# Kernel tuning notes

Measured on AMD Instinct MI355X. Metric: run time of the kernel, lower is better.

## Reference

```python
import jax, jax.numpy as jnp
import numpy as np
import math

B, T, C, NH, LEVEL = 2, 2048, 1024, 16, 3


def _build_sets(T, level):
    # hierarchical dyadic sets: levels `level`..floor(log2(T)), step 2^l
    sets = []
    levelmax = int(math.floor(math.log2(T)))
    for l in range(level, levelmax + 1):
        step = 2 ** l
        for i in range(T // step):
            sets.append((i * step, (i + 1) * step - 1))
    b = np.asarray(sets, dtype=np.int32)
    return b[:, 0], b[:, 1]


def setup_inputs() -> dict:
    key = jax.random.key(0)
    kx, kw1, kw2 = jax.random.split(key, 3)
    x = jax.random.normal(kx, (B, T, C), dtype=jnp.float32)
    # torch nn.Linear stores weight as (out_features, in_features); y = x @ W.T
    W_attn = jax.random.normal(kw1, (3 * C, C), dtype=jnp.float32) * (C ** -0.5)
    W_proj = jax.random.normal(kw2, (C, C), dtype=jnp.float32) * (C ** -0.5)
    return {"x": x, "W_attn": W_attn, "W_proj": W_proj}


def _get_slice(xc, l_idx, r_idx):
    # xc: (B,NH,T,hs) cumulative sums; returns sum over [l_idx, r_idx]
    r = xc[:, :, r_idx, :]
    l = xc[:, :, l_idx - 1, :] * (l_idx >= 1)[None, None, :, None].astype(xc.dtype)
    return r - l


def _forward(x, W_attn, W_proj):
    hs = C // NH
    scale = hs ** -0.5
    qkv = x @ W_attn.T                      # (B,T,3C)
    q, k, v = jnp.split(qkv, 3, axis=2)
    heads = lambda t: t.reshape(B, T, NH, hs).transpose(0, 2, 1, 3)  # (B,NH,T,hs)
    q, k, v = heads(q), heads(k), heads(v)
    phi = lambda t: jax.nn.elu(t) + 1.0     # feature_map = 'elu_plus'
    q_phi, k_phi = phi(q), phi(k)
    k_cum = jnp.cumsum(k_phi, axis=2)
    v_cum = jnp.cumsum(v, axis=2)

    l_np, r_np = _build_sets(T, LEVEL)
    l_idx, r_idx = jnp.asarray(l_np), jnp.asarray(r_np)
    K = _get_slice(k_cum, l_idx, r_idx)     # (B,NH,S,hs)
    V = _get_slice(v_cum, l_idx, r_idx)

    t_idx = jnp.arange(T)
    mask = t_idx[:, None] >= r_idx[None, :]                 # (T,S)
    logits = jnp.einsum('bhtd,bhsd->bhts', q, K) * scale    # raw q here (as in source)
    logits = jnp.where(mask[None, None], logits, -jnp.inf)

    # tail term over last (t mod 2^level)+1 tokens, uses q_phi
    Lmin = 2 ** LEVEL
    tail_len = t_idx % Lmin + 1
    l_tail = t_idx - tail_len + 1
    K_tail = _get_slice(k_cum, l_tail, t_idx)               # (B,NH,T,hs)
    V_tail = _get_slice(v_cum, l_tail, t_idx)
    tail_logit = jnp.sum(q_phi * K_tail, axis=-1) * scale   # (B,NH,T)

    full = jnp.concatenate([logits, tail_logit[..., None]], axis=-1)
    att = jax.nn.softmax(full, axis=-1)
    out = jnp.einsum('bhts,bhsd->bhtd', att[..., :-1], V) + att[..., -1:] * V_tail
    out = out.transpose(0, 2, 1, 3).reshape(B, T, C)
    return out @ W_proj.T


def reference(x, W_attn, W_proj):
    return _forward(x, W_attn, W_proj)
```

## Files before the change

kernel.cpp:

```cpp
#include <hip/hip_runtime.h>
#include <hip/hip_bf16.h>
#include <stdint.h>

#define B_    2
#define T_    2048
#define CD    1024
#define NH_   16
#define HS_   64
#define NSETS 511
#define NSP   512
#define QKV_LD 3072
#define NEGBIG (-3.4e38f)

typedef __attribute__((ext_vector_type(8))) short  short8;
typedef __attribute__((ext_vector_type(4))) float  f32x4;

__device__ __forceinline__ unsigned short f2bf(float f) {
  unsigned u = __float_as_uint(f);
  unsigned r = 0x7FFFu + ((u >> 16) & 1u);
  return (unsigned short)((u + r) >> 16);
}
__device__ __forceinline__ float bf2f(unsigned short h) {
  return __uint_as_float(((unsigned)h) << 16);
}
__device__ __forceinline__ float elu1(float x) {
  return x > 0.f ? x + 1.f : __expf(x);
}
__device__ __forceinline__ void gload16(const unsigned short* g, short* l) {
  __builtin_amdgcn_global_load_lds(
      (const __attribute__((address_space(1))) unsigned int*)g,
      (__attribute__((address_space(3))) unsigned int*)l, 16, 0, 0);
}

__global__ __launch_bounds__(256) void split3_kernel(
    const float* __restrict__ x, const float* __restrict__ Wa,
    const float* __restrict__ Wp,
    unsigned short* __restrict__ xh, unsigned short* __restrict__ xl,
    unsigned short* __restrict__ wah, unsigned short* __restrict__ wal,
    unsigned short* __restrict__ wph) {
  int bid = blockIdx.x;
  const float* src; unsigned short *hi, *lo; int base;
  if (bid < 16384)      { src = x;  hi = xh;  lo = xl;  base = bid; }
  else if (bid < 24576) { src = Wa; hi = wah; lo = wal; base = bid - 16384; }
  else if (bid < 28672) { src = Wa; hi = wah; lo = nullptr; base = bid - 16384; }
  else                  { src = Wp; hi = wph; lo = nullptr; base = bid - 28672; }
  int i = base * 256 + threadIdx.x;
  float v = src[i];
  unsigned short h = f2bf(v);
  hi[i] = h;
  if (lo) lo[i] = f2bf(v - bf2f(h));
}

template<int SPLIT>
__global__ __launch_bounds__(256) void gemm_bt(
    const unsigned short* __restrict__ Ah, const unsigned short* __restrict__ Al,
    const unsigned short* __restrict__ Bh, const unsigned short* __restrict__ Bl,
    float* __restrict__ Cmat, int M, int N, int K, int ldc)
{
  constexpr int NT = SPLIT ? 4 : 2;
  __shared__ short lds[NT * 4096];

  const int nwg = gridDim.x;
  const int cpx = nwg >> 3;
  const int bid = blockIdx.x;
  const int swb = (bid & 7) * cpx + (bid >> 3);
  const int nbx = N >> 7;
  const int bx = swb % nbx;
  const int by = swb / nbx;

  const int row0 = by * 128;
  const int col0 = bx * 128;
  const int tid  = threadIdx.x;
  const int lane = tid & 63;
  const int w    = tid >> 6;
  const int wr   = w >> 1, wc = w & 1;

  f32x4 acc[4][4];
  #pragma unroll
  for (int a = 0; a < 4; ++a)
    #pragma unroll
    for (int b = 0; b < 4; ++b)
      acc[a][b] = (f32x4){0.f, 0.f, 0.f, 0.f};

  const int rlane = lane & 15;
  const int kgrp  = lane >> 4;
  const int rsw   = (kgrp ^ (rlane & 3) ^ ((rlane >> 2) & 3)) << 4;

  const int slr = lane >> 2;
  const int sch = (lane & 3) ^ (slr & 3) ^ ((slr >> 2) & 3);

  const unsigned short* ssrc;
  size_t srb;
  short* sbase;
  if (SPLIT) {
    ssrc = (w == 0) ? Ah : (w == 1) ? Bh : (w == 2) ? Al : Bl;
    srb  = (w & 1) ? (size_t)col0 : (size_t)row0;
    sbase = &lds[w * 4096];
  } else {
    ssrc = (w & 1) ? Bh : Ah;
    srb  = (w & 1) ? (size_t)col0 : (size_t)row0;
    sbase = &lds[(w & 1) * 4096 + (w >> 1) * 2048];
    srb += (size_t)(w >> 1) * 64;
  }

  for (int kt = 0; kt < K; kt += 32) {
    __syncthreads();
    const unsigned short* g0 = ssrc + (srb + slr) * K + kt + (sch << 3);
    if (SPLIT) {
      #pragma unroll
      for (int i = 0; i < 8; ++i)
        gload16(g0 + (size_t)i * 16 * K, sbase + i * 512);
    } else {
      #pragma unroll
      for (int i = 0; i < 4; ++i)
        gload16(g0 + (size_t)i * 16 * K, sbase + i * 512);
    }
    __syncthreads();

    short8 aH[4], bH[4], aL[4], bL[4];
    #pragma unroll
    for (int m = 0; m < 4; ++m) {
      int r    = wr * 64 + m * 16 + rlane;
      int cidx = wc * 64 + m * 16 + rlane;
      aH[m] = *(const short8*)((const char*)lds + r * 64 + rsw);
      bH[m] = *(const short8*)((const char*)lds + 8192 + cidx * 64 + rsw);
      if (SPLIT) {
        aL[m] = *(const short8*)((const char*)lds + 16384 + r * 64 + rsw);
        bL[m] = *(const short8*)((const char*)lds + 24576 + cidx * 64 + rsw);
      }
    }
    #pragma unroll
    for (int mm = 0; mm < 4; ++mm)
      #pragma unroll
      for (int nn = 0; nn < 4; ++nn) {
        acc[mm][nn] = __builtin_amdgcn_mfma_f32_16x16x32_bf16(aH[mm], bH[nn], acc[mm][nn], 0, 0, 0);
        if (SPLIT) {
          acc[mm][nn] = __builtin_amdgcn_mfma_f32_16x16x32_bf16(aH[mm], bL[nn], acc[mm][nn], 0, 0, 0);
          acc[mm][nn] = __builtin_amdgcn_mfma_f32_16x16x32_bf16(aL[mm], bH[nn], acc[mm][nn], 0, 0, 0);
        }
      }
  }

  const int rl = (lane >> 4) * 4;
  const int cl = lane & 15;
  #pragma unroll
  for (int mm = 0; mm < 4; ++mm)
    #pragma unroll
    for (int nn = 0; nn < 4; ++nn)
      #pragma unroll
      for (int r = 0; r < 4; ++r) {
        int row = row0 + wr * 64 + mm * 16 + rl + r;
        int col = col0 + wc * 64 + nn * 16 + cl;
        Cmat[(size_t)row * ldc + col] = acc[mm][nn][r];
      }
}

__global__ __launch_bounds__(256) void cs_part(const float* __restrict__ qkv,
                                               float* __restrict__ part) {
  int blk = blockIdx.x;
  int q   = blk & 1;
  int seg = (blk >> 1) & 31;
  int b   = blk >> 6;
  int c   = threadIdx.x * 4;
  const float* src = qkv + (size_t)(b * T_ + seg * 64) * QKV_LD + CD + q * CD + c;
  float4 s = {0.f, 0.f, 0.f, 0.f};
  #pragma unroll 4
  for (int j = 0; j < 64; ++j) {
    float4 v = *(const float4*)(src + (size_t)j * QKV_LD);
    if (q == 0) {
      s.x += elu1(v.x); s.y += elu1(v.y); s.z += elu1(v.z); s.w += elu1(v.w);
    } else {
      s.x += v.x; s.y += v.y; s.z += v.z; s.w += v.w;
    }
  }
  *(float4*)(part + ((size_t)(b * 32 + seg) * 2048) + q * 1024 + c) = s;
}

__global__ void cs_prefix(float* __restrict__ part) {
  int idx = blockIdx.x * 256 + threadIdx.x;
  int b  = idx >> 11;
  int cc = idx & 2047;
  float run = 0.f;
  #pragma unroll 8
  for (int s = 0; s < 32; ++s) {
    size_t o = (size_t)(b * 32 + s) * 2048 + cc;
    float t = part[o];
    part[o] = run;
    run += t;
  }
}

__global__ __launch_bounds__(256) void cs_final(const float* __restrict__ qkv,
                                                const float* __restrict__ part,
                                                float* __restrict__ kcum,
                                                float* __restrict__ vcum) {
  int blk = blockIdx.x;
  int q   = blk & 1;
  int seg = (blk >> 1) & 31;
  int b   = blk >> 6;
  int c   = threadIdx.x * 4;
  int h   = c >> 6, d = c & 63;
  const float* src = qkv + (size_t)(b * T_ + seg * 64) * QKV_LD + CD + q * CD + c;
  float* dst = (q == 0 ? kcum : vcum) + ((size_t)(b * NH_ + h) * T_ + seg * 64) * HS_ + d;
  float4 s = *(const float4*)(part + ((size_t)(b * 32 + seg) * 2048) + q * 1024 + c);
  #pragma unroll 4
  for (int j = 0; j < 64; ++j) {
    float4 v = *(const float4*)(src + (size_t)j * QKV_LD);
    if (q == 0) {
      s.x += elu1(v.x); s.y += elu1(v.y); s.z += elu1(v.z); s.w += elu1(v.w);
    } else {
      s.x += v.x; s.y += v.y; s.z += v.z; s.w += v.w;
    }
    *(float4*)(dst + (size_t)j * HS_) = s;
  }
}

__global__ void build_sets(const float* __restrict__ kcum, const float* __restrict__ vcum,
                           unsigned short* __restrict__ Ksh, unsigned short* __restrict__ Ksl,
                           float* __restrict__ Vs, int* __restrict__ r_srt) {
  int idx = blockIdx.x * 256 + threadIdx.x;
  if (idx >= B_ * NH_ * NSP * HS_) return;
  int d  = idx & 63;
  int s  = (idx >> 6) & (NSP - 1);
  int bh = idx >> (6 + 9);
  if (s == NSETS) {
    size_t o = ((size_t)(bh << 9) + s) * HS_ + d;
    Ksh[o] = 0; Ksl[o] = 0; Vs[o] = 0.f;
    if (bh == 0 && d == 0) r_srt[s] = 0x7fffffff;
    return;
  }
  int lvl = 3, base = 0;
  while (s >= base + (T_ >> lvl)) { base += T_ >> lvl; ++lvl; }
  int i  = s - base;
  int m  = (i + 1) << lvl;
  int r  = m - 1;
  int li = i << lvl;
  int rank = lvl - 3;
  #pragma unroll
  for (int j = 3; j <= 11; ++j) rank += (m - 8) >> j;

  size_t rowr = ((size_t)bh * T_ + r) * HS_ + d;
  float kr = kcum[rowr], vr = vcum[rowr];
  if (li > 0) {
    size_t rowl = ((size_t)bh * T_ + li - 1) * HS_ + d;
    kr -= kcum[rowl];
    vr -= vcum[rowl];
  }
  size_t o = ((size_t)(bh << 9) + rank) * HS_ + d;
  unsigned short kh = f2bf(kr);
  Ksh[o] = kh;
  Ksl[o] = f2bf(kr - bf2f(kh));
  Vs[o]  = vr;
  if (bh == 0 && d == 0) r_srt[rank] = r;
}

__global__ __launch_bounds__(256) void vst_transpose(
    const float* __restrict__ Vs, unsigned short* __restrict__ Vst) {
  __shared__ float tile[64][65];
  int bh = blockIdx.x >> 3;
  int s0 = (blockIdx.x & 7) * 64;
  int tid = threadIdx.x;
  int srow = tid >> 2, c0 = (tid & 3) * 16;
  const float* src = Vs + ((size_t)(bh << 9) + s0 + srow) * HS_ + c0;
  #pragma unroll
  for (int j = 0; j < 4; ++j) {
    float4 v = *(const float4*)(src + j * 4);
    tile[srow][c0 + j*4 + 0] = v.x; tile[srow][c0 + j*4 + 1] = v.y;
    tile[srow][c0 + j*4 + 2] = v.z; tile[srow][c0 + j*4 + 3] = v.w;
  }
  __syncthreads();
  int d = tid >> 2, sq = (tid & 3) * 16;
  short8 a, b;
  #pragma unroll
  for (int j = 0; j < 8; ++j) {
    a[j] = (short)f2bf(tile[sq + j][d]);
    b[j] = (short)f2bf(tile[sq + 8 + j][d]);
  }
  unsigned short* dst = Vst + ((size_t)(bh << 6) + d) * NSP + s0 + sq;
  *(short8*)dst = a;
  *(short8*)(dst + 8) = b;
}

__global__ __launch_bounds__(256) void attn_mfma(
    const float* __restrict__ qkv, const float* __restrict__ kcum,
    const float* __restrict__ vcum,
    const unsigned short* __restrict__ Ksh, const unsigned short* __restrict__ Ksl,
    const unsigned short* __restrict__ Vst, const int* __restrict__ r_srt,
    unsigned short* __restrict__ attnb)
{
  __shared__ short Qh[64 * 64];
  __shared__ short Ql[64 * 64];
  __shared__ short Pl[4 * 16 * 64];
  __shared__ short KV[3 * 4096];
  __shared__ int   rs_lds[NSP];

  const int blk = blockIdx.x;
  const int xcd = blk & 7;
  const int j   = blk >> 3;
  const int bh  = xcd * 4 + (j >> 5);
  const int tch = (j + ((j >> 5) << 3)) & 31;
  const int b = bh >> 4, h = bh & 15;
  const int t0 = tch * 64;
  const int tid = threadIdx.x;
  const int lane = tid & 63;
  const int w = tid >> 6;
  const int col = lane & 15;
  const float scale = 0.125f;

  const int srow = lane >> 3;
  const int scsw = ((lane & 7) ^ srow) * 8;

  auto stage_tile = [&](short* kv, int s0) {
    #pragma unroll
    for (int L = w * 6; L < w * 6 + 6; ++L) {
      int a = L >> 3, i = L & 7;
      const unsigned short* src;
      if (a == 0)      src = Ksh + ((size_t)(bh << 9) + s0 + i * 8 + srow) * 64 + scsw;
      else if (a == 1) src = Ksl + ((size_t)(bh << 9) + s0 + i * 8 + srow) * 64 + scsw;
      else             src = Vst + ((size_t)(bh << 6) + i * 8 + srow) * NSP + s0 + scsw;
      gload16(src, kv + a * 4096 + i * 512 + lane * 8);
    }
  };

  int nmax = 0;
  #pragma unroll
  for (int jj = 3; jj <= 11; ++jj) nmax += (t0 + 64) >> jj;
  const int ntiles = (nmax + 63) >> 6;

  {
    int row = tid >> 2;
    int d0  = (tid & 3) * 16;
    const float* qr = qkv + (size_t)(b * T_ + t0 + row) * QKV_LD + h * HS_ + d0;
    float qv[16];
    #pragma unroll
    for (int jj = 0; jj < 4; ++jj) {
      float4 v = *(const float4*)(qr + jj * 4);
      qv[jj*4+0] = v.x; qv[jj*4+1] = v.y; qv[jj*4+2] = v.z; qv[jj*4+3] = v.w;
    }
    short8 hh[2], ll[2];
    #pragma unroll
    for (int c = 0; c < 2; ++c)
      #pragma unroll
      for (int jj = 0; jj < 8; ++jj) {
        float f = qv[c*8+jj];
        unsigned short hi = f2bf(f);
        hh[c][jj] = (short)hi;
        ll[c][jj] = (short)f2bf(f - bf2f(hi));
      }
    int swz = (row & 7) << 4;
    #pragma unroll
    for (int c = 0; c < 2; ++c) {
      int addr = (row * 128 + d0 * 2 + c * 16) ^ swz;
      *(short8*)((char*)Qh + addr) = hh[c];
      *(short8*)((char*)Ql + addr) = ll[c];
    }
    for (int s = tid; s < NSP; s += 256) rs_lds[s] = r_srt[s];
  }

  int rows[4];
  #pragma unroll
  for (int r = 0; r < 4; ++r) rows[r] = t0 + w * 16 + (lane >> 4) * 4 + r;

  f32x4 O[4];
  #pragma unroll
  for (int f = 0; f < 4; ++f) O[f] = (f32x4){0.f, 0.f, 0.f, 0.f};
  float mrun[4] = {NEGBIG, NEGBIG, NEGBIG, NEGBIG};
  float lsum[4] = {0.f, 0.f, 0.f, 0.f};

  const int arow  = w * 16 + col;
  const int aswz  = (arow & 7) << 4;
  const int kgrp  = (lane >> 4) * 8;

  for (int tile = 0; tile < ntiles; ++tile) {
    const int s0 = tile * 64;
    stage_tile(KV, s0);
    __syncthreads();

    const char* kc = (const char*)KV;
    f32x4 S[4];
    #pragma unroll
    for (int f = 0; f < 4; ++f) S[f] = (f32x4){0.f, 0.f, 0.f, 0.f};

    #pragma unroll
    for (int ks = 0; ks < 2; ++ks) {
      int abyte = (arow * 128 + (kgrp + ks * 32) * 2) ^ aswz;
      short8 aH = *(const short8*)((const char*)Qh + abyte);
      short8 aL = *(const short8*)((const char*)Ql + abyte);
      int chnk = (lane >> 4) + ks * 4;
      #pragma unroll
      for (int f = 0; f < 4; ++f) {
        int so = f * 16 + col;
        int kb = so * 128 + ((chnk ^ (so & 7)) << 4);
        short8 bHv = *(const short8*)(kc + kb);
        short8 bLv = *(const short8*)(kc + 8192 + kb);
        S[f] = __builtin_amdgcn_mfma_f32_16x16x32_bf16(aH, bHv, S[f], 0, 0, 0);
        S[f] = __builtin_amdgcn_mfma_f32_16x16x32_bf16(aH, bLv, S[f], 0, 0, 0);
        S[f] = __builtin_amdgcn_mfma_f32_16x16x32_bf16(aL, bHv, S[f], 0, 0, 0);
      }
    }

    int rsv[4];
    #pragma unroll
    for (int f = 0; f < 4; ++f) rsv[f] = rs_lds[s0 + f * 16 + col];

    float zv[4][4];
    #pragma unroll
    for (int f = 0; f < 4; ++f)
      #pragma unroll
      for (int r = 0; r < 4; ++r)
        zv[f][r] = (rsv[f] > rows[r]) ? NEGBIG : S[f][r] * scale;

    float mx[4];
    #pragma unroll
    for (int r = 0; r < 4; ++r)
      mx[r] = fmaxf(fmaxf(zv[0][r], zv[1][r]), fmaxf(zv[2][r], zv[3][r]));
    int pred = (mx[0] <= mrun[0] + 8.f) & (mx[1] <= mrun[1] + 8.f) &
               (mx[2] <= mrun[2] + 8.f) & (mx[3] <= mrun[3] + 8.f);
    if (!__all(pred)) {
      #pragma unroll
      for (int r = 0; r < 4; ++r) {
        float mt = mx[r];
        mt = fmaxf(mt, __shfl_xor(mt, 1));
        mt = fmaxf(mt, __shfl_xor(mt, 2));
        mt = fmaxf(mt, __shfl_xor(mt, 4));
        mt = fmaxf(mt, __shfl_xor(mt, 8));
        float mv = fmaxf(mrun[r], mt);
        float fs = __expf(mrun[r] - mv);
        lsum[r] *= fs;
        #pragma unroll
        for (int f = 0; f < 4; ++f) O[f][r] *= fs;
        mrun[r] = mv;
      }
    }

    char* pw = (char*)Pl + w * 2048;
    #pragma unroll
    for (int r = 0; r < 4; ++r) {
      int rowr = (lane >> 4) * 4 + r;
      int rswz = (rowr & 7) << 4;
      #pragma unroll
      for (int f = 0; f < 4; ++f) {
        float p = __expf(zv[f][r] - mrun[r]);
        p = (rsv[f] > rows[r]) ? 0.f : p;
        lsum[r] += p;
        int addr = (rowr * 128 + (f * 16 + col) * 2) ^ rswz;
        *(unsigned short*)(pw + addr) = f2bf(p);
      }
    }

    #pragma unroll
    for (int ks = 0; ks < 2; ++ks) {
      int pbyte = (col * 128 + (kgrp + ks * 32) * 2) ^ ((col & 7) << 4);
      short8 pa = *(const short8*)(pw + pbyte);
      int chnk = (lane >> 4) + ks * 4;
      #pragma unroll
      for (int f = 0; f < 4; ++f) {
        int dr = f * 16 + col;
        short8 bv = *(const short8*)(kc + 16384 + dr * 128 + ((chnk ^ (dr & 7)) << 4));
        O[f] = __builtin_amdgcn_mfma_f32_16x16x32_bf16(pa, bv, O[f], 0, 0, 0);
      }
    }

    __syncthreads();
  }

  float lrun[4];
  #pragma unroll
  for (int r = 0; r < 4; ++r) {
    float l = lsum[r];
    l += __shfl_xor(l, 1);
    l += __shfl_xor(l, 2);
    l += __shfl_xor(l, 4);
    l += __shfl_xor(l, 8);
    lrun[r] = l;
  }

  float ztail;
  {
    int trow = lane >> 2;
    int t = t0 + w * 16 + trow;
    int d0 = (lane & 3) * 16;
    const float* qr = qkv + (size_t)(b * T_ + t) * QKV_LD + h * HS_ + d0;
    float qv[16];
    #pragma unroll
    for (int jj = 0; jj < 4; ++jj) {
      float4 v = *(const float4*)(qr + jj * 4);
      qv[jj*4+0] = v.x; qv[jj*4+1] = v.y; qv[jj*4+2] = v.z; qv[jj*4+3] = v.w;
    }
    int lt = t & ~7;
    const float* kc1 = kcum + ((size_t)bh * T_ + t) * HS_ + d0;
    float kt[16];
    if (lt > 0) {
      const float* kc0 = kcum + ((size_t)bh * T_ + (lt - 1)) * HS_ + d0;
      #pragma unroll
      for (int jj = 0; jj < 16; ++jj) kt[jj] = kc1[jj] - kc0[jj];
    } else {
      #pragma unroll
      for (int jj = 0; jj < 16; ++jj) kt[jj] = kc1[jj];
    }
    float z = 0.f;
    #pragma unroll
    for (int jj = 0; jj < 16; ++jj) {
      float qp = qv[jj] > 0.f ? qv[jj] + 1.f : __expf(qv[jj]);
      z += qp * kt[jj];
    }
    z += __shfl_xor(z, 1);
    z += __shfl_xor(z, 2);
    ztail = z * scale;
  }

  #pragma unroll
  for (int r = 0; r < 4; ++r) {
    float zt = __shfl(ztail, ((lane >> 4) * 4 + r) * 4);
    float mv = fmaxf(mrun[r], zt);
    float fs = __expf(mrun[r] - mv);
    float pwgt = __expf(zt - mv);
    lrun[r] = lrun[r] * fs + pwgt;
    int tr = rows[r];
    int ltr = tr & ~7;
    #pragma unroll
    for (int f = 0; f < 4; ++f) {
      int d = f * 16 + col;
      float v1 = vcum[((size_t)bh * T_ + tr) * HS_ + d];
      float vt = (ltr > 0) ? v1 - vcum[((size_t)bh * T_ + (ltr - 1)) * HS_ + d] : v1;
      O[f][r] = O[f][r] * fs + pwgt * vt;
    }
  }

  #pragma unroll
  for (int r = 0; r < 4; ++r) {
    float inv = 1.f / lrun[r];
    unsigned short* orow = attnb + (size_t)(b * T_ + rows[r]) * CD + h * HS_;
    #pragma unroll
    for (int f = 0; f < 4; ++f)
      orow[f * 16 + col] = f2bf(O[f][r] * inv);
  }
}

extern "C" void kernel_launch(void* const* d_in, const int* in_sizes, int n_in,
                              void* d_out, int out_size, void* d_ws, size_t ws_size,
                              hipStream_t stream) {
  const float* x  = (const float*)d_in[0];
  const float* Wa = (const float*)d_in[1];
  const float* Wp = (const float*)d_in[2];
  float* out = (float*)d_out;

  char* ws = (char*)d_ws;
  size_t off = 0;
  auto alloc = [&](size_t bytes) -> char* {
    char* p = ws + off;
    off += (bytes + 255) & ~(size_t)255;
    return p;
  };

  const int M = B_ * T_;
  float* qkv  = (float*)alloc((size_t)M * QKV_LD * 4);
  float* kcum = (float*)alloc((size_t)B_ * NH_ * T_ * HS_ * 4);
  float* vcum = (float*)alloc((size_t)B_ * NH_ * T_ * HS_ * 4);
  float* part = (float*)alloc((size_t)B_ * 32 * 2048 * 4);
  unsigned short* wph = (unsigned short*)alloc((size_t)CD * CD * 2);

  char* regionA = alloc((size_t)16777216);
  unsigned short* xh = (unsigned short*)regionA;
  unsigned short* xl = (unsigned short*)(regionA + (size_t)M * CD * 2);
  const size_t SETS_ELEMS = (size_t)B_ * NH_ * NSP * HS_;
  unsigned short* Ksh = (unsigned short*)regionA;
  unsigned short* Ksl = Ksh + SETS_ELEMS;
  float*          Vss = (float*)(regionA + 2 * SETS_ELEMS * 2);
  unsigned short* Vst = (unsigned short*)(regionA + 2 * SETS_ELEMS * 2 + SETS_ELEMS * 4);
  int*            r_srt = (int*)(regionA + 2 * SETS_ELEMS * 2 + SETS_ELEMS * 4 + SETS_ELEMS * 2);

  char* regionB = alloc((size_t)12582912);
  unsigned short* wah = (unsigned short*)regionB;
  unsigned short* wal = (unsigned short*)(regionB + (size_t)3 * CD * CD * 2);
  unsigned short* attnb = (unsigned short*)regionB;

  split3_kernel<<<dim3(32768), dim3(256), 0, stream>>>(
      x, Wa, Wp, xh, xl, wah, wal, wph);

  gemm_bt<1><<<dim3((2048 / 128) * (M / 128)), dim3(256), 0, stream>>>(
      xh, xl, wah, wal, qkv, M, 2048, CD, QKV_LD);

  gemm_bt<0><<<dim3((1024 / 128) * (M / 128)), dim3(256), 0, stream>>>(
      xh, (const unsigned short*)nullptr, wah + (size_t)2048 * CD,
      (const unsigned short*)nullptr, qkv + 2048, M, 1024, CD, QKV_LD);

  cs_part<<<dim3(B_ * 32 * 2), dim3(256), 0, stream>>>(qkv, part);
  cs_prefix<<<dim3(B_ * 2048 / 256), dim3(256), 0, stream>>>(part);
  cs_final<<<dim3(B_ * 32 * 2), dim3(256), 0, stream>>>(qkv, part, kcum, vcum);

  build_sets<<<dim3((B_ * NH_ * NSP * HS_) / 256), dim3(256), 0, stream>>>(
      kcum, vcum, Ksh, Ksl, Vss, r_srt);
  vst_transpose<<<dim3(B_ * NH_ * (NSP / 64)), dim3(256), 0, stream>>>(Vss, Vst);

  attn_mfma<<<dim3(B_ * NH_ * (T_ / 64)), dim3(256), 0, stream>>>(
      qkv, kcum, vcum, Ksh, Ksl, Vst, r_srt, attnb);

  gemm_bt<0><<<dim3((CD / 128) * (M / 128)), dim3(256), 0, stream>>>(
      attnb, (const unsigned short*)nullptr, wph, (const unsigned short*)nullptr,
      out, M, CD, CD, CD);
}
```

Measured before the change: 223.8 us.

## Fuse QKV GEMMs, double cumsum segments, and widen attention row tiles

Merges the split and non-split QKV GEMM launches into one kernel that interleaves both tile types across 768 blocks. The cumsum now uses 64 segments of 32 rows for more parallelism, and the prefix step holds its values in registers. The attention kernel processes 128 query rows per block, 32 per wave, and keeps Q in registers instead of LDS, so each staged K/V tile is reused across twice as many rows. This cuts launch count and K/V staging traffic at the cost of higher register pressure and half as many attention blocks.

```diff
diff --git a/kernel.cpp b/kernel.cpp
--- a/kernel.cpp
+++ b/kernel.cpp
@@ -52,24 +52,12 @@
 }
 
 template<int SPLIT>
-__global__ __launch_bounds__(256) void gemm_bt(
+__device__ __forceinline__ void gemm_body(
+    short* lds,
     const unsigned short* __restrict__ Ah, const unsigned short* __restrict__ Al,
     const unsigned short* __restrict__ Bh, const unsigned short* __restrict__ Bl,
-    float* __restrict__ Cmat, int M, int N, int K, int ldc)
+    float* __restrict__ Cmat, int K, int ldc, int row0, int col0)
 {
-  constexpr int NT = SPLIT ? 4 : 2;
-  __shared__ short lds[NT * 4096];
-
-  const int nwg = gridDim.x;
-  const int cpx = nwg >> 3;
-  const int bid = blockIdx.x;
-  const int swb = (bid & 7) * cpx + (bid >> 3);
-  const int nbx = N >> 7;
-  const int bx = swb % nbx;
-  const int by = swb / nbx;
-
-  const int row0 = by * 128;
-  const int col0 = bx * 128;
   const int tid  = threadIdx.x;
   const int lane = tid & 63;
   const int w    = tid >> 6;
@@ -155,17 +143,56 @@
       }
 }
 
+__global__ __launch_bounds__(256) void gemm_qkv(
+    const unsigned short* __restrict__ xh, const unsigned short* __restrict__ xl,
+    const unsigned short* __restrict__ wah, const unsigned short* __restrict__ wal,
+    float* __restrict__ qkv)
+{
+  __shared__ short lds[4 * 4096];
+  int bid = blockIdx.x;
+  int t3  = bid % 3;
+  if (t3 < 2) {
+    int s = (bid / 3) * 2 + t3;
+    int bx = s & 15, by = s >> 4;
+    gemm_body<1>(lds, xh, xl, wah, wal, qkv,
+                 CD, QKV_LD, by * 128, bx * 128);
+  } else {
+    int p = bid / 3;
+    int bx = p & 7, by = p >> 3;
+    gemm_body<0>(lds, xh, nullptr, wah + (size_t)2048 * CD, nullptr,
+                 qkv + 2048, CD, QKV_LD, by * 128, bx * 128);
+  }
+}
+
+template<int SPLIT>
+__global__ __launch_bounds__(256) void gemm_bt(
+    const unsigned short* __restrict__ Ah, const unsigned short* __restrict__ Al,
+    const unsigned short* __restrict__ Bh, const unsigned short* __restrict__ Bl,
+    float* __restrict__ Cmat, int M, int N, int K, int ldc)
+{
+  constexpr int NT = SPLIT ? 4 : 2;
+  __shared__ short lds[NT * 4096];
+  const int nwg = gridDim.x;
+  const int cpx = nwg >> 3;
+  const int bid = blockIdx.x;
+  const int swb = (bid & 7) * cpx + (bid >> 3);
+  const int nbx = N >> 7;
+  const int bx = swb % nbx;
+  const int by = swb / nbx;
+  gemm_body<SPLIT>(lds, Ah, Al, Bh, Bl, Cmat, K, ldc, by * 128, bx * 128);
+}
+
 __global__ __launch_bounds__(256) void cs_part(const float* __restrict__ qkv,
                                                float* __restrict__ part) {
   int blk = blockIdx.x;
   int q   = blk & 1;
-  int seg = (blk >> 1) & 31;
-  int b   = blk >> 6;
+  int seg = (blk >> 1) & 63;
+  int b   = blk >> 7;
   int c   = threadIdx.x * 4;
-  const float* src = qkv + (size_t)(b * T_ + seg * 64) * QKV_LD + CD + q * CD + c;
+  const float* src = qkv + (size_t)(b * T_ + seg * 32) * QKV_LD + CD + q * CD + c;
   float4 s = {0.f, 0.f, 0.f, 0.f};
   #pragma unroll 4
-  for (int j = 0; j < 64; ++j) {
+  for (int j = 0; j < 32; ++j) {
     float4 v = *(const float4*)(src + (size_t)j * QKV_LD);
     if (q == 0) {
       s.x += elu1(v.x); s.y += elu1(v.y); s.z += elu1(v.z); s.w += elu1(v.w);
@@ -173,21 +200,21 @@
       s.x += v.x; s.y += v.y; s.z += v.z; s.w += v.w;
     }
   }
-  *(float4*)(part + ((size_t)(b * 32 + seg) * 2048) + q * 1024 + c) = s;
+  *(float4*)(part + ((size_t)(b * 64 + seg) * 2048) + q * 1024 + c) = s;
 }
 
 __global__ void cs_prefix(float* __restrict__ part) {
   int idx = blockIdx.x * 256 + threadIdx.x;
   int b  = idx >> 11;
   int cc = idx & 2047;
+  float v[64];
+  #pragma unroll
+  for (int s = 0; s < 64; ++s) v[s] = part[(size_t)(b * 64 + s) * 2048 + cc];
   float run = 0.f;
-  #pragma unroll 8
-  for (int s = 0; s < 32; ++s) {
-    size_t o = (size_t)(b * 32 + s) * 2048 + cc;
-    float t = part[o];
-    part[o] = run;
-    run += t;
-  }
+  #pragma unroll
+  for (int s = 0; s < 64; ++s) { float t = v[s]; v[s] = run; run += t; }
+  #pragma unroll
+  for (int s = 0; s < 64; ++s) part[(size_t)(b * 64 + s) * 2048 + cc] = v[s];
 }
 
 __global__ __launch_bounds__(256) void cs_final(const float* __restrict__ qkv,
@@ -196,15 +223,15 @@
                                                 float* __restrict__ vcum) {
   int blk = blockIdx.x;
   int q   = blk & 1;
-  int seg = (blk >> 1) & 31;
-  int b   = blk >> 6;
+  int seg = (blk >> 1) & 63;
+  int b   = blk >> 7;
   int c   = threadIdx.x * 4;
   int h   = c >> 6, d = c & 63;
-  const float* src = qkv + (size_t)(b * T_ + seg * 64) * QKV_LD + CD + q * CD + c;
-  float* dst = (q == 0 ? kcum : vcum) + ((size_t)(b * NH_ + h) * T_ + seg * 64) * HS_ + d;
-  float4 s = *(const float4*)(part + ((size_t)(b * 32 + seg) * 2048) + q * 1024 + c);
+  const float* src = qkv + (size_t)(b * T_ + seg * 32) * QKV_LD + CD + q * CD + c;
+  float* dst = (q == 0 ? kcum : vcum) + ((size_t)(b * NH_ + h) * T_ + seg * 32) * HS_ + d;
+  float4 s = *(const float4*)(part + ((size_t)(b * 64 + seg) * 2048) + q * 1024 + c);
   #pragma unroll 4
-  for (int j = 0; j < 64; ++j) {
+  for (int j = 0; j < 32; ++j) {
     float4 v = *(const float4*)(src + (size_t)j * QKV_LD);
     if (q == 0) {
       s.x += elu1(v.x); s.y += elu1(v.y); s.z += elu1(v.z); s.w += elu1(v.w);
@@ -288,29 +315,29 @@
     const unsigned short* __restrict__ Vst, const int* __restrict__ r_srt,
     unsigned short* __restrict__ attnb)
 {
-  __shared__ short Qh[64 * 64];
-  __shared__ short Ql[64 * 64];
-  __shared__ short Pl[4 * 16 * 64];
+  __shared__ short Pl[4 * 2048];
   __shared__ short KV[3 * 4096];
   __shared__ int   rs_lds[NSP];
 
   const int blk = blockIdx.x;
   const int xcd = blk & 7;
   const int j   = blk >> 3;
-  const int bh  = xcd * 4 + (j >> 5);
-  const int tch = (j + ((j >> 5) << 3)) & 31;
+  const int bhx = j >> 4;
+  const int bh  = xcd * 4 + bhx;
+  const int rb  = ((j & 15) + bhx * 4) & 15;
   const int b = bh >> 4, h = bh & 15;
-  const int t0 = tch * 64;
+  const int t0 = rb * 128;
   const int tid = threadIdx.x;
   const int lane = tid & 63;
   const int w = tid >> 6;
   const int col = lane & 15;
+  const int kgrp = (lane >> 4) * 8;
   const float scale = 0.125f;
 
   const int srow = lane >> 3;
   const int scsw = ((lane & 7) ^ srow) * 8;
 
-  auto stage_tile = [&](short* kv, int s0) {
+  auto stage_tile = [&](int s0) {
     #pragma unroll
     for (int L = w * 6; L < w * 6 + 6; ++L) {
       int a = L >> 3, i = L & 7;
@@ -318,84 +345,78 @@
       if (a == 0)      src = Ksh + ((size_t)(bh << 9) + s0 + i * 8 + srow) * 64 + scsw;
       else if (a == 1) src = Ksl + ((size_t)(bh << 9) + s0 + i * 8 + srow) * 64 + scsw;
       else             src = Vst + ((size_t)(bh << 6) + i * 8 + srow) * NSP + s0 + scsw;
-      gload16(src, kv + a * 4096 + i * 512 + lane * 8);
+      gload16(src, KV + a * 4096 + i * 512 + lane * 8);
     }
   };
 
+  short8 qh[2][2], ql[2][2];
+  #pragma unroll
+  for (int rr = 0; rr < 2; ++rr) {
+    int qrow = t0 + w * 32 + rr * 16 + col;
+    const float* qr = qkv + (size_t)(b * T_ + qrow) * QKV_LD + h * HS_;
+    #pragma unroll
+    for (int ks = 0; ks < 2; ++ks) {
+      float4 v0 = *(const float4*)(qr + kgrp + ks * 32);
+      float4 v1 = *(const float4*)(qr + kgrp + ks * 32 + 4);
+      float vv[8] = {v0.x, v0.y, v0.z, v0.w, v1.x, v1.y, v1.z, v1.w};
+      #pragma unroll
+      for (int jj = 0; jj < 8; ++jj) {
+        unsigned short hi = f2bf(vv[jj]);
+        qh[rr][ks][jj] = (short)hi;
+        ql[rr][ks][jj] = (short)f2bf(vv[jj] - bf2f(hi));
+      }
+    }
+  }
+  for (int s = tid; s < NSP; s += 256) rs_lds[s] = r_srt[s];
+
+  int rows[2][4];
+  #pragma unroll
+  for (int rr = 0; rr < 2; ++rr)
+    #pragma unroll
+    for (int r = 0; r < 4; ++r)
+      rows[rr][r] = t0 + w * 32 + rr * 16 + (lane >> 4) * 4 + r;
+
+  f32x4 O[2][4];
+  float mrun[2][4], lsum[2][4];
+  #pragma unroll
+  for (int rr = 0; rr < 2; ++rr)
+    #pragma unroll
+    for (int f = 0; f < 4; ++f) {
+      O[rr][f] = (f32x4){0.f, 0.f, 0.f, 0.f};
+      mrun[rr][f] = NEGBIG; lsum[rr][f] = 0.f;
+    }
+
   int nmax = 0;
   #pragma unroll
-  for (int jj = 3; jj <= 11; ++jj) nmax += (t0 + 64) >> jj;
+  for (int jj = 3; jj <= 11; ++jj) nmax += (t0 + 128) >> jj;
   const int ntiles = (nmax + 63) >> 6;
-
-  {
-    int row = tid >> 2;
-    int d0  = (tid & 3) * 16;
-    const float* qr = qkv + (size_t)(b * T_ + t0 + row) * QKV_LD + h * HS_ + d0;
-    float qv[16];
-    #pragma unroll
-    for (int jj = 0; jj < 4; ++jj) {
-      float4 v = *(const float4*)(qr + jj * 4);
-      qv[jj*4+0] = v.x; qv[jj*4+1] = v.y; qv[jj*4+2] = v.z; qv[jj*4+3] = v.w;
-    }
-    short8 hh[2], ll[2];
-    #pragma unroll
-    for (int c = 0; c < 2; ++c)
-      #pragma unroll
-      for (int jj = 0; jj < 8; ++jj) {
-        float f = qv[c*8+jj];
-        unsigned short hi = f2bf(f);
-        hh[c][jj] = (short)hi;
-        ll[c][jj] = (short)f2bf(f - bf2f(hi));
-      }
-    int swz = (row & 7) << 4;
-    #pragma unroll
-    for (int c = 0; c < 2; ++c) {
-      int addr = (row * 128 + d0 * 2 + c * 16) ^ swz;
-      *(short8*)((char*)Qh + addr) = hh[c];
-      *(short8*)((char*)Ql + addr) = ll[c];
-    }
-    for (int s = tid; s < NSP; s += 256) rs_lds[s] = r_srt[s];
-  }
-
-  int rows[4];
-  #pragma unroll
-  for (int r = 0; r < 4; ++r) rows[r] = t0 + w * 16 + (lane >> 4) * 4 + r;
-
-  f32x4 O[4];
-  #pragma unroll
-  for (int f = 0; f < 4; ++f) O[f] = (f32x4){0.f, 0.f, 0.f, 0.f};
-  float mrun[4] = {NEGBIG, NEGBIG, NEGBIG, NEGBIG};
-  float lsum[4] = {0.f, 0.f, 0.f, 0.f};
-
-  const int arow  = w * 16 + col;
-  const int aswz  = (arow & 7) << 4;
-  const int kgrp  = (lane >> 4) * 8;
 
   for (int tile = 0; tile < ntiles; ++tile) {
     const int s0 = tile * 64;
-    stage_tile(KV, s0);
+    stage_tile(s0);
     __syncthreads();
 
-    const char* kc = (const char*)KV;
-    f32x4 S[4];
-    #pragma unroll
-    for (int f = 0; f < 4; ++f) S[f] = (f32x4){0.f, 0.f, 0.f, 0.f};
+    f32x4 S[2][4];
+    #pragma unroll
+    for (int rr = 0; rr < 2; ++rr)
+      #pragma unroll
+      for (int f = 0; f < 4; ++f) S[rr][f] = (f32x4){0.f, 0.f, 0.f, 0.f};
 
     #pragma unroll
     for (int ks = 0; ks < 2; ++ks) {
-      int abyte = (arow * 128 + (kgrp + ks * 32) * 2) ^ aswz;
-      short8 aH = *(const short8*)((const char*)Qh + abyte);
-      short8 aL = *(const short8*)((const char*)Ql + abyte);
       int chnk = (lane >> 4) + ks * 4;
       #pragma unroll
       for (int f = 0; f < 4; ++f) {
         int so = f * 16 + col;
         int kb = so * 128 + ((chnk ^ (so & 7)) << 4);
-        short8 bHv = *(const short8*)(kc + kb);
-        short8 bLv = *(const short8*)(kc + 8192 + kb);
-        S[f] = __builtin_amdgcn_mfma_f32_16x16x32_bf16(aH, bHv, S[f], 0, 0, 0);
-        S[f] = __builtin_amdgcn_mfma_f32_16x16x32_bf16(aH, bLv, S[f], 0, 0, 0);
-        S[f] = __builtin_amdgcn_mfma_f32_16x16x32_bf16(aL, bHv, S[f], 0, 0, 0);
+        short8 bHv = *(const short8*)((const char*)KV + kb);
+        short8 bLv = *(const short8*)((const char*)KV + 8192 + kb);
+        #pragma unroll
+        for (int rr = 0; rr < 2; ++rr) {
+          S[rr][f] = __builtin_amdgcn_mfma_f32_16x16x32_bf16(qh[rr][ks], bHv, S[rr][f], 0, 0, 0);
+          S[rr][f] = __builtin_amdgcn_mfma_f32_16x16x32_bf16(qh[rr][ks], bLv, S[rr][f], 0, 0, 0);
+          S[rr][f] = __builtin_amdgcn_mfma_f32_16x16x32_bf16(ql[rr][ks], bHv, S[rr][f], 0, 0, 0);
+        }
       }
     }
 
@@ -403,82 +424,96 @@
     #pragma unroll
     for (int f = 0; f < 4; ++f) rsv[f] = rs_lds[s0 + f * 16 + col];
 
-    float zv[4][4];
-    #pragma unroll
-    for (int f = 0; f < 4; ++f)
-      #pragma unroll
-      for (int r = 0; r < 4; ++r)
-        zv[f][r] = (rsv[f] > rows[r]) ? NEGBIG : S[f][r] * scale;
-
-    float mx[4];
-    #pragma unroll
-    for (int r = 0; r < 4; ++r)
-      mx[r] = fmaxf(fmaxf(zv[0][r], zv[1][r]), fmaxf(zv[2][r], zv[3][r]));
-    int pred = (mx[0] <= mrun[0] + 8.f) & (mx[1] <= mrun[1] + 8.f) &
-               (mx[2] <= mrun[2] + 8.f) & (mx[3] <= mrun[3] + 8.f);
+    #pragma unroll
+    for (int rr = 0; rr < 2; ++rr)
+      #pragma unroll
+      for (int f = 0; f < 4; ++f)
+        #pragma unroll
+        for (int r = 0; r < 4; ++r)
+          S[rr][f][r] = (rsv[f] > rows[rr][r]) ? NEGBIG : S[rr][f][r] * scale;
+
+    float mx[2][4];
+    int pred = 1;
+    #pragma unroll
+    for (int rr = 0; rr < 2; ++rr)
+      #pragma unroll
+      for (int r = 0; r < 4; ++r) {
+        mx[rr][r] = fmaxf(fmaxf(S[rr][0][r], S[rr][1][r]),
+                          fmaxf(S[rr][2][r], S[rr][3][r]));
+        pred &= (mx[rr][r] <= mrun[rr][r] + 8.f);
+      }
     if (!__all(pred)) {
       #pragma unroll
+      for (int rr = 0; rr < 2; ++rr)
+        #pragma unroll
+        for (int r = 0; r < 4; ++r) {
+          float mt = mx[rr][r];
+          mt = fmaxf(mt, __shfl_xor(mt, 1));
+          mt = fmaxf(mt, __shfl_xor(mt, 2));
+          mt = fmaxf(mt, __shfl_xor(mt, 4));
+          mt = fmaxf(mt, __shfl_xor(mt, 8));
+          float mv = fmaxf(mrun[rr][r], mt);
+          float fs = __expf(mrun[rr][r] - mv);
+          lsum[rr][r] *= fs;
+          #pragma unroll
+          for (int f = 0; f < 4; ++f) O[rr][f][r] *= fs;
+          mrun[rr][r] = mv;
+        }
+    }
+
+    char* pw = (char*)Pl + w * 4096;
+    #pragma unroll
+    for (int rr = 0; rr < 2; ++rr)
+      #pragma unroll
       for (int r = 0; r < 4; ++r) {
-        float mt = mx[r];
-        mt = fmaxf(mt, __shfl_xor(mt, 1));
-        mt = fmaxf(mt, __shfl_xor(mt, 2));
-        mt = fmaxf(mt, __shfl_xor(mt, 4));
-        mt = fmaxf(mt, __shfl_xor(mt, 8));
-        float mv = fmaxf(mrun[r], mt);
-        float fs = __expf(mrun[r] - mv);
-        lsum[r] *= fs;
+        int rowr = rr * 16 + (lane >> 4) * 4 + r;
+        int rswz = (rowr & 7) << 4;
         #pragma unroll
-        for (int f = 0; f < 4; ++f) O[f][r] *= fs;
-        mrun[r] = mv;
-      }
-    }
-
-    char* pw = (char*)Pl + w * 2048;
-    #pragma unroll
-    for (int r = 0; r < 4; ++r) {
-      int rowr = (lane >> 4) * 4 + r;
-      int rswz = (rowr & 7) << 4;
-      #pragma unroll
-      for (int f = 0; f < 4; ++f) {
-        float p = __expf(zv[f][r] - mrun[r]);
-        p = (rsv[f] > rows[r]) ? 0.f : p;
-        lsum[r] += p;
-        int addr = (rowr * 128 + (f * 16 + col) * 2) ^ rswz;
-        *(unsigned short*)(pw + addr) = f2bf(p);
-      }
-    }
+        for (int f = 0; f < 4; ++f) {
+          float p = __expf(S[rr][f][r] - mrun[rr][r]);
+          p = (rsv[f] > rows[rr][r]) ? 0.f : p;
+          lsum[rr][r] += p;
+          int addr = (rowr * 128 + (f * 16 + col) * 2) ^ rswz;
+          *(unsigned short*)(pw + addr) = f2bf(p);
+        }
+      }
 
     #pragma unroll
     for (int ks = 0; ks < 2; ++ks) {
-      int pbyte = (col * 128 + (kgrp + ks * 32) * 2) ^ ((col & 7) << 4);
-      short8 pa = *(const short8*)(pw + pbyte);
       int chnk = (lane >> 4) + ks * 4;
+      int pb0 = (col * 128 + (kgrp + ks * 32) * 2) ^ ((col & 7) << 4);
+      short8 pa0 = *(const short8*)(pw + pb0);
+      short8 pa1 = *(const short8*)(pw + 2048 + pb0);
       #pragma unroll
       for (int f = 0; f < 4; ++f) {
         int dr = f * 16 + col;
-        short8 bv = *(const short8*)(kc + 16384 + dr * 128 + ((chnk ^ (dr & 7)) << 4));
-        O[f] = __builtin_amdgcn_mfma_f32_16x16x32_bf16(pa, bv, O[f], 0, 0, 0);
+        short8 bv = *(const short8*)((const char*)KV + 16384 + dr * 128 + ((chnk ^ (dr & 7)) << 4));
+        O[0][f] = __builtin_amdgcn_mfma_f32_16x16x32_bf16(pa0, bv, O[0][f], 0, 0, 0);
+        O[1][f] = __builtin_amdgcn_mfma_f32_16x16x32_bf16(pa1, bv, O[1][f], 0, 0, 0);
       }
     }
 
     __syncthreads();
   }
 
-  float lrun[4];
-  #pragma unroll
-  for (int r = 0; r < 4; ++r) {
-    float l = lsum[r];
-    l += __shfl_xor(l, 1);
-    l += __shfl_xor(l, 2);
-    l += __shfl_xor(l, 4);
-    l += __shfl_xor(l, 8);
-    lrun[r] = l;
-  }
-
-  float ztail;
-  {
+  float lrun[2][4];
+  #pragma unroll
+  for (int rr = 0; rr < 2; ++rr)
+    #pragma unroll
+    for (int r = 0; r < 4; ++r) {
+      float l = lsum[rr][r];
+      l += __shfl_xor(l, 1);
+      l += __shfl_xor(l, 2);
+      l += __shfl_xor(l, 4);
+      l += __shfl_xor(l, 8);
+      lrun[rr][r] = l;
+    }
+
+  float ztail[2];
+  #pragma unroll
+  for (int rr = 0; rr < 2; ++rr) {
     int trow = lane >> 2;
-    int t = t0 + w * 16 + trow;
+    int t = t0 + w * 32 + rr * 16 + trow;
     int d0 = (lane & 3) * 16;
     const float* qr = qkv + (size_t)(b * T_ + t) * QKV_LD + h * HS_ + d0;
     float qv[16];
@@ -506,35 +541,39 @@
     }
     z += __shfl_xor(z, 1);
     z += __shfl_xor(z, 2);
-    ztail = z * scale;
-  }
-
-  #pragma unroll
-  for (int r = 0; r < 4; ++r) {
-    float zt = __shfl(ztail, ((lane >> 4) * 4 + r) * 4);
-    float mv = fmaxf(mrun[r], zt);
-    float fs = __expf(mrun[r] - mv);
-    float pwgt = __expf(zt - mv);
-    lrun[r] = lrun[r] * fs + pwgt;
-    int tr = rows[r];
-    int ltr = tr & ~7;
-    #pragma unroll
-    for (int f = 0; f < 4; ++f) {
-      int d = f * 16 + col;
-      float v1 = vcum[((size_t)bh * T_ + tr) * HS_ + d];
-      float vt = (ltr > 0) ? v1 - vcum[((size_t)bh * T_ + (ltr - 1)) * HS_ + d] : v1;
-      O[f][r] = O[f][r] * fs + pwgt * vt;
-    }
-  }
-
-  #pragma unroll
-  for (int r = 0; r < 4; ++r) {
-    float inv = 1.f / lrun[r];
-    unsigned short* orow = attnb + (size_t)(b * T_ + rows[r]) * CD + h * HS_;
-    #pragma unroll
-    for (int f = 0; f < 4; ++f)
-      orow[f * 16 + col] = f2bf(O[f][r] * inv);
-  }
+    ztail[rr] = z * scale;
+  }
+
+  #pragma unroll
+  for (int rr = 0; rr < 2; ++rr)
+    #pragma unroll
+    for (int r = 0; r < 4; ++r) {
+      float zt = __shfl(ztail[rr], ((lane >> 4) * 4 + r) * 4);
+      float mv = fmaxf(mrun[rr][r], zt);
+      float fs = __expf(mrun[rr][r] - mv);
+      float pwgt = __expf(zt - mv);
+      lrun[rr][r] = lrun[rr][r] * fs + pwgt;
+      int tr = rows[rr][r];
+      int ltr = tr & ~7;
+      #pragma unroll
+      for (int f = 0; f < 4; ++f) {
+        int d = f * 16 + col;
+        float v1 = vcum[((size_t)bh * T_ + tr) * HS_ + d];
+        float vt = (ltr > 0) ? v1 - vcum[((size_t)bh * T_ + (ltr - 1)) * HS_ + d] : v1;
+        O[rr][f][r] = O[rr][f][r] * fs + pwgt * vt;
+      }
+    }
+
+  #pragma unroll
+  for (int rr = 0; rr < 2; ++rr)
+    #pragma unroll
+    for (int r = 0; r < 4; ++r) {
+      float inv = 1.f / lrun[rr][r];
+      unsigned short* orow = attnb + (size_t)(b * T_ + rows[rr][r]) * CD + h * HS_;
+      #pragma unroll
+      for (int f = 0; f < 4; ++f)
+        orow[f * 16 + col] = f2bf(O[rr][f][r] * inv);
+    }
 }
 
 extern "C" void kernel_launch(void* const* d_in, const int* in_sizes, int n_in,
@@ -557,7 +596,7 @@
   float* qkv  = (float*)alloc((size_t)M * QKV_LD * 4);
   float* kcum = (float*)alloc((size_t)B_ * NH_ * T_ * HS_ * 4);
   float* vcum = (float*)alloc((size_t)B_ * NH_ * T_ * HS_ * 4);
-  float* part = (float*)alloc((size_t)B_ * 32 * 2048 * 4);
+  float* part = (float*)alloc((size_t)B_ * 64 * 2048 * 4);
   unsigned short* wph = (unsigned short*)alloc((size_t)CD * CD * 2);
 
   char* regionA = alloc((size_t)16777216);
@@ -578,22 +617,17 @@
   split3_kernel<<<dim3(32768), dim3(256), 0, stream>>>(
       x, Wa, Wp, xh, xl, wah, wal, wph);
 
-  gemm_bt<1><<<dim3((2048 / 128) * (M / 128)), dim3(256), 0, stream>>>(
-      xh, xl, wah, wal, qkv, M, 2048, CD, QKV_LD);
-
-  gemm_bt<0><<<dim3((1024 / 128) * (M / 128)), dim3(256), 0, stream>>>(
-      xh, (const unsigned short*)nullptr, wah + (size_t)2048 * CD,
-      (const unsigned short*)nullptr, qkv + 2048, M, 1024, CD, QKV_LD);
-
-  cs_part<<<dim3(B_ * 32 * 2), dim3(256), 0, stream>>>(qkv, part);
+  gemm_qkv<<<dim3(768), dim3(256), 0, stream>>>(xh, xl, wah, wal, qkv);
+
+  cs_part<<<dim3(B_ * 64 * 2), dim3(256), 0, stream>>>(qkv, part);
   cs_prefix<<<dim3(B_ * 2048 / 256), dim3(256), 0, stream>>>(part);
-  cs_final<<<dim3(B_ * 32 * 2), dim3(256), 0, stream>>>(qkv, part, kcum, vcum);
+  cs_final<<<dim3(B_ * 64 * 2), dim3(256), 0, stream>>>(qkv, part, kcum, vcum);
 
   build_sets<<<dim3((B_ * NH_ * NSP * HS_) / 256), dim3(256), 0, stream>>>(
       kcum, vcum, Ksh, Ksl, Vss, r_srt);
   vst_transpose<<<dim3(B_ * NH_ * (NSP / 64)), dim3(256), 0, stream>>>(Vss, Vst);
 
-  attn_mfma<<<dim3(B_ * NH_ * (T_ / 64)), dim3(256), 0, stream>>>(
+  attn_mfma<<<dim3(512), dim3(256), 0, stream>>>(
       qkv, kcum, vcum, Ksh, Ksl, Vst, r_srt, attnb);
 
   gemm_bt<0><<<dim3((CD / 128) * (M / 128)), dim3(256), 0, stream>>>(
```

Result: slower. 241.4 us (+7.8%).
